# Kernel tuning notes

Hardware: AMD Instinct MI355X
Metric: run time of the kernel (lower is better)

Reference implementation:

```python
import jax, jax.numpy as jnp
import numpy as np
from jax import lax

K, E, HID, NH, L = 512, 256, 512, 8, 2
N, S1, S2, C, U, V, W = 2, 8, 9, 3, 8, 8, 8
S = S1 + S2 - 1  # 16, matches sum(cfg['seq_length']) - 1


def setup_inputs() -> dict:
    key = jax.random.key(0)
    ks = iter(jax.random.split(key, 40))
    g = lambda shape, s=0.02: jax.random.normal(next(ks), shape, jnp.float32) * s
    inp = {
        'code': jax.random.randint(next(ks), (N, S1, C, U, V, W), 0, K),
        'ncode': jax.random.randint(next(ks), (N, S2, C, U, V, W), 0, K),
        'emb': g((K, E)), 'pos_emb': g((S, E)),
        'Wq': g((L, 3, 3, 3, E, E)), 'bq': g((L, E)),
        'Wk': g((L, 3, 3, 3, E, E)), 'bk': g((L, E)),
        'Wv': g((L, 3, 3, 3, E, E)), 'bv': g((L, E)),
        'Wo': g((L, 3, 3, 3, E, E)), 'bo': g((L, E)),
        'ln1_g': jnp.ones((L, E)), 'ln1_b': jnp.zeros((L, E)),
        'ln2_g': jnp.ones((L, E)), 'ln2_b': jnp.zeros((L, E)),
        'Wc1': g((L, 3, 3, 3, E, HID)), 'bc1': g((L, HID)),
        'Wc2': g((L, 3, 3, 3, HID, E)), 'bc2': g((L, E)),
        'cls_W1': g((E, E)), 'cls_b1': jnp.zeros((E,)),
        'cls_ln_g': jnp.ones((E,)), 'cls_ln_b': jnp.zeros((E,)),
        'cls_W2': g((E, K)), 'cls_b2': jnp.zeros((K,)),
    }
    return inp


def _conv3d(t, w, b):
    # t: [B, S, U, V, W, Cin]; conv with kernel 3, stride 1, pad 1 (SAME)
    B_, S_, U_, V_, W_, Ci = t.shape
    y = lax.conv_general_dilated(t.reshape(B_ * S_, U_, V_, W_, Ci), w, (1, 1, 1), 'SAME',
                                 dimension_numbers=('NDHWC', 'DHWIO', 'NDHWC')) + b
    return y.reshape(B_, S_, U_, V_, W_, -1)


def _ln(t, g, b):
    mu = t.mean(-1, keepdims=True)
    var = ((t - mu) ** 2).mean(-1, keepdims=True)
    return (t - mu) * lax.rsqrt(var + 1e-5) * g + b


def _forward(code, ncode, emb, pos_emb, Wq, bq, Wk, bk, Wv, bv, Wo, bo,
             ln1_g, ln1_b, ln2_g, ln2_b, Wc1, bc1, Wc2, bc2,
             cls_W1, cls_b1, cls_ln_g, cls_ln_b, cls_W2, cls_b2):
    x = jnp.concatenate([code, ncode[:, :-1]], axis=1)  # [N, S, C, U, V, W]
    n, s, c, u, v, w = x.shape
    s2 = ncode.shape[1]
    x = x.transpose(0, 2, 1, 3, 4, 5).reshape(n * c, s, u, v, w)
    h = emb[x] + pos_emb[:s][None, :, None, None, None, :]  # [B, S, U, V, W, E]
    e = h.shape[-1]
    d = e // NH
    scale = jnp.asarray(d, h.dtype) ** 0.5
    # causal mask with first seq_length[0] columns fully visible
    m = jnp.tril(jnp.ones((s, s), bool)).at[:, :S1].set(True)

    def heads(t):
        return t.reshape(t.shape[0], s, u, v, w, NH, d).transpose(0, 5, 2, 3, 4, 1, 6)

    for i in range(Wq.shape[0]):
        q = heads(_conv3d(h, Wq[i], bq[i]))
        kk = heads(_conv3d(h, Wk[i], bk[i]))
        vv = heads(_conv3d(h, Wv[i], bv[i]))
        scores = jnp.einsum('bnuvwsd,bnuvwtd->bnuvwst', q, kk) / scale
        scores = jnp.where(m, scores, jnp.asarray(-1e30, scores.dtype))
        attn = jax.nn.softmax(scores, axis=-1)
        o = jnp.einsum('bnuvwst,bnuvwtd->bnuvwsd', attn, vv)
        o = o.transpose(0, 5, 2, 3, 4, 1, 6).reshape(h.shape[0], s, u, v, w, e)
        o = _conv3d(o, Wo[i], bo[i])
        h = _ln(h + o, ln1_g[i], ln1_b[i])
        f = _conv3d(jax.nn.gelu(_conv3d(h, Wc1[i], bc1[i]), approximate=False), Wc2[i], bc2[i])
        h = _ln(h + f, ln2_g[i], ln2_b[i])

    h = h[:, -s2:]
    h = h.reshape(n, c, s2, u, v, w, e).transpose(0, 2, 1, 3, 4, 5, 6)  # [N, S2, C, U, V, W, E]
    z = jnp.einsum('...e,ef->...f', h, cls_W1) + cls_b1
    z = jax.nn.gelu(_ln(z, cls_ln_g, cls_ln_b), approximate=False)
    z = jnp.einsum('...e,ek->...k', z, cls_W2) + cls_b2
    score = z.transpose(0, 6, 1, 2, 3, 4, 5)  # [N, K, S2, C, U, V, W]
    return score


def reference(code, ncode, emb, pos_emb, Wq, bq, Wk, bk, Wv, bv, Wo, bo,
              ln1_g, ln1_b, ln2_g, ln2_b, Wc1, bc1, Wc2, bc2,
              cls_W1, cls_b1, cls_ln_g, cls_ln_b, cls_W2, cls_b2):
    score = _forward(code, ncode, emb, pos_emb, Wq, bq, Wk, bk, Wv, bv, Wo, bo,
                     ln1_g, ln1_b, ln2_g, ln2_b, Wc1, bc1, Wc2, bc2,
                     cls_W1, cls_b1, cls_ln_g, cls_ln_b, cls_W2, cls_b2)
    logp = jax.nn.log_softmax(score, axis=1)
    nll = -jnp.take_along_axis(logp, ncode[:, None], axis=1)[:, 0]
    loss = nll.mean()
    pred = jnp.argmax(score, axis=1)
    return score, loss, pred
```

## Files before the change

### kernel.cpp

```cpp
#include <hip/hip_runtime.h>


typedef _Float16 f16;
typedef __attribute__((ext_vector_type(8))) _Float16 f16x8;
typedef __attribute__((ext_vector_type(4))) _Float16 f16x4;
typedef __attribute__((ext_vector_type(4))) float f32x4;

static constexpr long kSC = 14155776;
static constexpr float kDS = 4.8828125e-4f;

#define MFMA16(a, b, c) __builtin_amdgcn_mfma_f32_16x16x32_f16((a), (b), (c), 0, 0, 0)

__device__ __forceinline__ void gl16(const void* g, void* l) {
  __builtin_amdgcn_global_load_lds((const __attribute__((address_space(1))) void*)g,
                                   (__attribute__((address_space(3))) void*)l,
                                   16, 0, 0);
}

__device__ __forceinline__ float wave_sum_f(float x) {
#pragma unroll
  for (int m = 32; m; m >>= 1) x += __shfl_xor(x, m);
  return x;
}

__device__ __forceinline__ void split2(float x, f16* h, f16* l) {
  f16 hh = (f16)x;
  *h = hh;
  *l = (f16)((x - (float)hh) * 2048.0f);
}

__device__ __forceinline__ float rec2(f16 h, f16 l) {
  return (float)h + (float)l * kDS;
}

__device__ __forceinline__ float gelu_exact(float x) {
  return 0.5f * x * (1.0f + erff(x * 0.70710678118654752f));
}

__global__ __launch_bounds__(256) void wsplit_kernel(
    const float* __restrict__ src, f16* __restrict__ hi, f16* __restrict__ lo,
    int G, int Ci, int Co, int CoTot, int co0) {
  long n = (long)G * Ci * Co;
  long i = (long)blockIdx.x * 256 + threadIdx.x;
  if (i >= n) return;
  int co = (int)(i % Co);
  long t = i / Co;
  int ci = (int)(t % Ci);
  int g  = (int)(t / Ci);
  float x = src[i];
  long o = ((long)g * CoTot + co0 + co) * Ci + ci;
  split2(x, hi + o, lo + o);
}

__global__ __launch_bounds__(256) void bpack_kernel(
    const float* __restrict__ bq, const float* __restrict__ bk,
    const float* __restrict__ bv, float* __restrict__ dst) {
  int i = blockIdx.x * 256 + threadIdx.x;
  if (i < 256) dst[i] = bq[i];
  else if (i < 512) dst[i] = bk[i - 256];
  else if (i < 768) dst[i] = bv[i - 512];
}

__global__ __launch_bounds__(256) void embed_kernel(
    const int* __restrict__ code, const int* __restrict__ ncode,
    const float* __restrict__ emb, const float* __restrict__ pos,
    f16* __restrict__ Hh, f16* __restrict__ Hl) {
  int tok = blockIdx.x;
  int e = threadIdx.x;
  int g = tok >> 13;
  int rem = tok & 8191;
  int s = rem >> 9;
  int vox = rem & 511;
  int n = g / 3, c = g - 3 * n;
  int idx;
  if (s < 8) idx = code[((n * 8 + s) * 3 + c) * 512 + vox];
  else       idx = ncode[((n * 9 + (s - 8)) * 3 + c) * 512 + vox];
  float val = emb[idx * 256 + e] + pos[s * 256 + e];
  long o = (long)tok * 256 + e;
  split2(val, Hh + o, Hl + o);
}

template <int CIN, int COUTT, int ACT, int RESID>
__global__ __launch_bounds__(256, 2) void conv4_kernel(
    const f16* __restrict__ Xh, const f16* __restrict__ Xl, long xz_s, int xr,
    const f16* __restrict__ Wh, const f16* __restrict__ Wl,
    const float* __restrict__ bias,
    f16* __restrict__ Yh, f16* __restrict__ Yl, long yz_s, int yr, int nz) {
  constexpr int KB = CIN / 32;
  constexpr int NY = COUTT / 128;
  __shared__ __align__(16) f16 lsAll[32768];

  const int nwg = 64 * NY * nz;
  const int q = nwg >> 3;
  const int bid = blockIdx.x;
  const int wg = (bid & 7) * q + (bid >> 3);
  const int y = wg / (64 * nz);
  const int rem = wg - y * (64 * nz);
  const int z = rem >> 6;
  const int mt = rem & 63;
  const int img = mt >> 2, up = mt & 3;
  const int u0 = up * 2;
  const int coutb0 = y * 128;

  const int tid = threadIdx.x;
  const int wid = tid >> 6, lane = tid & 63;
  const int wm = wid >> 1, wn = wid & 1;
  const int l15 = lane & 15, lk = lane >> 4;

  const long xz = (long)z * xz_s;
  const long yz = (long)z * yz_s;

  f32x4 aA[4][4], aB[4][4];
#pragma unroll
  for (int mf = 0; mf < 4; ++mf)
#pragma unroll
    for (int nf = 0; nf < 4; ++nf) {
      float bv = bias[coutb0 + wn * 64 + nf * 16 + l15];
      aA[mf][nf] = (f32x4){bv, bv, bv, bv};
      aB[mf][nf] = (f32x4){0.f, 0.f, 0.f, 0.f};
    }

  const int swrow = tid >> 2;
  const int sslot = tid & 3;
  const int sswz = sslot ^ ((tid >> 3) & 3);

  auto stageA = [&](int kb) {
#pragma unroll
    for (int j = 0; j < 4; ++j) {
      const int uu = u0 - 1 + j;
      if (uu < 0 || uu >= 8) continue;
      const long g = xz + ((long)(img * 512 + uu * 64 + swrow)) * (long)xr
                     + kb * 32 + sswz * 8;
      gl16(Xh + g, &lsAll[j * 2048 + tid * 8]);
      gl16(Xl + g, &lsAll[8192 + j * 2048 + tid * 8]);
    }
  };
  auto stageB = [&](int o, int kb, int buf) {
#pragma unroll
    for (int i = 0; i < 2; ++i) {
      const long g = ((long)o * COUTT + coutb0 + i * 64 + swrow) * (long)CIN
                     + kb * 32 + sswz * 8;
      gl16(Wh + g, &lsAll[16384 + (buf * 2 + 0) * 4096 + i * 2048 + tid * 8]);
      gl16(Wl + g, &lsAll[16384 + (buf * 2 + 1) * 4096 + i * 2048 + tid * 8]);
    }
  };
  auto compute = [&](int o, int buf) {
    const int du = o / 9 - 1, dv = (o / 3) % 3 - 1, dw = o % 3 - 1;
    f16x8 bh[4], bl[4];
#pragma unroll
    for (int nf = 0; nf < 4; ++nf) {
      const int rb = wn * 64 + nf * 16 + l15;
      const int sw = lk ^ ((rb >> 1) & 3);
      bh[nf] = *(const f16x8*)&lsAll[16384 + (buf * 2 + 0) * 4096 + rb * 32 + sw * 8];
      bl[nf] = *(const f16x8*)&lsAll[16384 + (buf * 2 + 1) * 4096 + rb * 32 + sw * 8];
    }
    const int gu = u0 + wm + du;
    const bool uok = (0 <= gu) && (gu < 8);
    const int p = wm + 1 + du;
#pragma unroll
    for (int mf = 0; mf < 4; ++mf) {
      const int vrow = mf * 16 + l15;
      const int vv = (vrow >> 3) + dv, ww = (vrow & 7) + dw;
      const bool ok = uok && ((unsigned)vv < 8u) && ((unsigned)ww < 8u);
      f16x8 ah = {0, 0, 0, 0, 0, 0, 0, 0};
      f16x8 al = {0, 0, 0, 0, 0, 0, 0, 0};
      if (ok) {
        const int lrow = p * 64 + vv * 8 + ww;
        const int sw = lk ^ ((lrow >> 1) & 3);
        ah = *(const f16x8*)&lsAll[lrow * 32 + sw * 8];
        al = *(const f16x8*)&lsAll[8192 + lrow * 32 + sw * 8];
      }
#pragma unroll
      for (int nf = 0; nf < 4; ++nf) {
        aA[mf][nf] = MFMA16(ah, bh[nf], aA[mf][nf]);
        aB[mf][nf] = MFMA16(ah, bl[nf], aB[mf][nf]);
        aB[mf][nf] = MFMA16(al, bh[nf], aB[mf][nf]);
      }
    }
  };

  stageA(0);
  stageB(0, 0, 0);
  __syncthreads();

  int cur = 0;
#pragma unroll 1
  for (int kb = 0; kb < KB; ++kb) {
#pragma unroll 1
    for (int o = 0; o < 27; ++o) {
      if (o < 26)           stageB(o + 1, kb, cur ^ 1);
      else if (kb + 1 < KB) stageB(0, kb + 1, cur ^ 1);
      compute(o, cur);
      __syncthreads();
      cur ^= 1;
    }
    if (kb + 1 < KB) {
      stageA(kb + 1);
      __syncthreads();
    }
  }

  float* sY = (float*)lsAll;
#pragma unroll 1
  for (int rh = 0; rh < 2; ++rh) {
    if (wm == rh) {
#pragma unroll
      for (int mf = 0; mf < 4; ++mf)
#pragma unroll
        for (int nf = 0; nf < 4; ++nf)
#pragma unroll
          for (int j = 0; j < 4; ++j) {
            const int row = mf * 16 + lk * 4 + j;
            const int col = wn * 64 + nf * 16 + l15;
            sY[row * 132 + col] = aA[mf][nf][j] + aB[mf][nf][j] * kDS;
          }
    }
    __syncthreads();
#pragma unroll
    for (int it = 0; it < 2; ++it) {
      const int row = it * 32 + (tid >> 3);
      const int c0 = (tid & 7) * 16;
      const long grow = (long)img * 512 + (u0 + rh) * 64 + row;
      const long gidx = yz + grow * (long)yr + coutb0 + c0;
      float yv[16];
#pragma unroll
      for (int i2 = 0; i2 < 16; ++i2) yv[i2] = sY[row * 132 + c0 + i2];
      if (ACT) {
#pragma unroll
        for (int i2 = 0; i2 < 16; ++i2) yv[i2] = gelu_exact(yv[i2]);
      }
      if (RESID) {
        f16x8 r0h = *(const f16x8*)&Yh[gidx];
        f16x8 r1h = *(const f16x8*)&Yh[gidx + 8];
        f16x8 r0l = *(const f16x8*)&Yl[gidx];
        f16x8 r1l = *(const f16x8*)&Yl[gidx + 8];
#pragma unroll
        for (int i2 = 0; i2 < 8; ++i2) {
          yv[i2] += rec2(r0h[i2], r0l[i2]);
          yv[8 + i2] += rec2(r1h[i2], r1l[i2]);
        }
      }
      f16x8 h0, h1, l0, l1;
#pragma unroll
      for (int i2 = 0; i2 < 8; ++i2) {
        f16 a, b;
        split2(yv[i2], &a, &b); h0[i2] = a; l0[i2] = b;
        split2(yv[8 + i2], &a, &b); h1[i2] = a; l1[i2] = b;
      }
      *(f16x8*)&Yh[gidx] = h0;
      *(f16x8*)&Yh[gidx + 8] = h1;
      *(f16x8*)&Yl[gidx] = l0;
      *(f16x8*)&Yl[gidx + 8] = l1;
    }
    __syncthreads();
  }
}

template <int K_, int COUT, bool F32OUT>
__global__ __launch_bounds__(256) void gemm_kernel(
    const f16* __restrict__ Xh, const f16* __restrict__ Xl,
    const f16* __restrict__ Wh, const f16* __restrict__ Wl,
    const float* __restrict__ bias,
    f16* __restrict__ Yh, f16* __restrict__ Yl, float* __restrict__ Yf) {
  const int m0 = blockIdx.x * 64;
  const int coutb = blockIdx.y * 64;
  const int tid = threadIdx.x;
  const int wid = tid >> 6, lane = tid & 63;
  const int l15 = lane & 15, lk = lane >> 4;
  const int arow = m0 + wid * 16 + l15;

  f32x4 accA[4], accB[4];
#pragma unroll
  for (int cg = 0; cg < 4; ++cg) {
    float bv = bias[coutb + cg * 16 + l15];
    accA[cg] = (f32x4){bv, bv, bv, bv};
    accB[cg] = (f32x4){0.f, 0.f, 0.f, 0.f};
  }
  const f16* pah = Xh + (long)arow * K_ + lk * 8;
  const f16* pal = Xl + (long)arow * K_ + lk * 8;
  const f16* pbh = Wh + ((long)coutb + l15) * K_ + lk * 8;
  const f16* pbl = Wl + ((long)coutb + l15) * K_ + lk * 8;
#pragma unroll 2
  for (int kb = 0; kb < K_ / 32; ++kb) {
    f16x8 ah = *(const f16x8*)(pah + kb * 32);
    f16x8 al = *(const f16x8*)(pal + kb * 32);
#pragma unroll
    for (int cg = 0; cg < 4; ++cg) {
      f16x8 bh = *(const f16x8*)(pbh + (long)cg * 16 * K_ + kb * 32);
      f16x8 bl = *(const f16x8*)(pbl + (long)cg * 16 * K_ + kb * 32);
      accA[cg] = MFMA16(ah, bh, accA[cg]);
      accB[cg] = MFMA16(ah, bl, accB[cg]);
      accB[cg] = MFMA16(al, bh, accB[cg]);
    }
  }
  const long ybase = ((long)m0 + wid * 16) * (long)COUT + coutb;
#pragma unroll
  for (int cg = 0; cg < 4; ++cg)
#pragma unroll
    for (int j = 0; j < 4; ++j) {
      int r = lk * 4 + j;
      float y = accA[cg][j] + accB[cg][j] * kDS;
      long idx = ybase + (long)r * COUT + cg * 16 + l15;
      if (F32OUT) Yf[idx] = y;
      else        split2(y, Yh + idx, Yl + idx);
    }
}

__global__ __launch_bounds__(256) void attn_kernel(
    f16* __restrict__ QKVh, f16* __restrict__ QKVl) {
  __shared__ float sq[4][16][33];
  __shared__ float sk[4][16][33];
  __shared__ float sv[4][16][33];
  __shared__ float ss[4][16][17];
  const int wid = threadIdx.x >> 6, lane = threadIdx.x & 63;
  const int p = blockIdx.x * 4 + wid;
  const int cs = p >> 12;
  const int loc = p & 4095;
  const int nh = loc >> 9;
  const int vox = loc & 511;
  const int srow = lane >> 2;
  const int dp = (lane & 3) * 8;
  const long sbase = (long)cs * 6291456;
  const long base = sbase + ((long)(srow * 512 + vox)) * 768 + nh * 32 + dp;

  {
    f16x8 qh = *(const f16x8*)(QKVh + base);
    f16x8 ql = *(const f16x8*)(QKVl + base);
    f16x8 kh = *(const f16x8*)(QKVh + base + 256);
    f16x8 kl = *(const f16x8*)(QKVl + base + 256);
    f16x8 vh = *(const f16x8*)(QKVh + base + 512);
    f16x8 vl = *(const f16x8*)(QKVl + base + 512);
#pragma unroll
    for (int j = 0; j < 8; ++j) {
      sq[wid][srow][dp + j] = rec2(qh[j], ql[j]);
      sk[wid][srow][dp + j] = rec2(kh[j], kl[j]);
      sv[wid][srow][dp + j] = rec2(vh[j], vl[j]);
    }
  }
  __syncthreads();
#pragma unroll
  for (int pp = 0; pp < 4; ++pp) {
    int pr = lane * 4 + pp;
    int qi = pr >> 4, kt = pr & 15;
    float s = 0.f;
#pragma unroll
    for (int d = 0; d < 32; ++d) s += sq[wid][qi][d] * sk[wid][kt][d];
    bool allowed = (kt < 8) || (kt <= qi);
    ss[wid][qi][kt] = allowed ? s * 0.17677669529663687f : -1e30f;
  }
  __syncthreads();
  if (lane < 16) {
    float m = -1e30f;
#pragma unroll
    for (int t = 0; t < 16; ++t) m = fmaxf(m, ss[wid][lane][t]);
    float ex[16];
    float sum = 0.f;
#pragma unroll
    for (int t = 0; t < 16; ++t) { ex[t] = expf(ss[wid][lane][t] - m); sum += ex[t]; }
    float inv = 1.0f / sum;
#pragma unroll
    for (int t = 0; t < 16; ++t) ss[wid][lane][t] = ex[t] * inv;
  }
  __syncthreads();
  float o[8] = {0, 0, 0, 0, 0, 0, 0, 0};
#pragma unroll
  for (int t = 0; t < 16; ++t) {
    float a = ss[wid][srow][t];
#pragma unroll
    for (int j = 0; j < 8; ++j) o[j] += a * sv[wid][t][dp + j];
  }
#pragma unroll
  for (int j = 0; j < 8; ++j) split2(o[j], QKVh + base + j, QKVl + base + j);
}

__global__ __launch_bounds__(256) void ln_kernel(
    f16* __restrict__ Hh, f16* __restrict__ Hl,
    const float* __restrict__ gam, const float* __restrict__ bet) {
  const int wid = threadIdx.x >> 6, lane = threadIdx.x & 63;
  const long tok = (long)blockIdx.x * 4 + wid;
  const long base = tok * 256 + lane * 4;
  f16x4 hh = *(const f16x4*)(Hh + base);
  f16x4 hl = *(const f16x4*)(Hl + base);
  float v0 = rec2(hh[0], hl[0]), v1 = rec2(hh[1], hl[1]);
  float v2 = rec2(hh[2], hl[2]), v3 = rec2(hh[3], hl[3]);
  float mu = wave_sum_f(v0 + v1 + v2 + v3) * (1.0f / 256.0f);
  float d0 = v0 - mu, d1 = v1 - mu, d2 = v2 - mu, d3 = v3 - mu;
  float var = wave_sum_f(d0 * d0 + d1 * d1 + d2 * d2 + d3 * d3) * (1.0f / 256.0f);
  float rs = rsqrtf(var + 1e-5f);
  float4 gv = *(const float4*)(gam + lane * 4);
  float4 bv = *(const float4*)(bet + lane * 4);
  float y0 = d0 * rs * gv.x + bv.x, y1 = d1 * rs * gv.y + bv.y;
  float y2 = d2 * rs * gv.z + bv.z, y3 = d3 * rs * gv.w + bv.w;
  f16x4 oh, ol;
  f16 a, b2;
  split2(y0, &a, &b2); oh[0] = a; ol[0] = b2;
  split2(y1, &a, &b2); oh[1] = a; ol[1] = b2;
  split2(y2, &a, &b2); oh[2] = a; ol[2] = b2;
  split2(y3, &a, &b2); oh[3] = a; ol[3] = b2;
  *(f16x4*)(Hh + base) = oh;
  *(f16x4*)(Hl + base) = ol;
}

__global__ __launch_bounds__(256) void ln_gelu_kernel(
    f16* __restrict__ Zh, f16* __restrict__ Zl,
    const float* __restrict__ gam, const float* __restrict__ bet) {
  const int wid = threadIdx.x >> 6, lane = threadIdx.x & 63;
  const long tok = (long)blockIdx.x * 4 + wid;
  const long base = tok * 256 + lane * 4;
  f16x4 hh = *(const f16x4*)(Zh + base);
  f16x4 hl = *(const f16x4*)(Zl + base);
  float v0 = rec2(hh[0], hl[0]), v1 = rec2(hh[1], hl[1]);
  float v2 = rec2(hh[2], hl[2]), v3 = rec2(hh[3], hl[3]);
  float mu = wave_sum_f(v0 + v1 + v2 + v3) * (1.0f / 256.0f);
  float d0 = v0 - mu, d1 = v1 - mu, d2 = v2 - mu, d3 = v3 - mu;
  float var = wave_sum_f(d0 * d0 + d1 * d1 + d2 * d2 + d3 * d3) * (1.0f / 256.0f);
  float rs = rsqrtf(var + 1e-5f);
  float4 gv = *(const float4*)(gam + lane * 4);
  float4 bv = *(const float4*)(bet + lane * 4);
  float y0 = gelu_exact(d0 * rs * gv.x + bv.x);
  float y1 = gelu_exact(d1 * rs * gv.y + bv.y);
  float y2 = gelu_exact(d2 * rs * gv.z + bv.z);
  float y3 = gelu_exact(d3 * rs * gv.w + bv.w);
  f16x4 oh, ol;
  f16 a, b2;
  split2(y0, &a, &b2); oh[0] = a; ol[0] = b2;
  split2(y1, &a, &b2); oh[1] = a; ol[1] = b2;
  split2(y2, &a, &b2); oh[2] = a; ol[2] = b2;
  split2(y3, &a, &b2); oh[3] = a; ol[3] = b2;
  *(f16x4*)(Zh + base) = oh;
  *(f16x4*)(Zl + base) = ol;
}

__global__ __launch_bounds__(256) void gather_kernel(
    const f16* __restrict__ Hh, const f16* __restrict__ Hl, int n,
    f16* __restrict__ Xh, f16* __restrict__ Xl) {
  const int tc = blockIdx.x;
  const int e = threadIdx.x;
  const int s2 = tc / 1536;
  int r = tc - s2 * 1536;
  const int c = r >> 9;
  const int vox = r & 511;
  const int g = n * 3 + c;
  const int s = 7 + s2;
  const long src = ((long)(g * 16 + s) * 512 + vox) * 256 + e;
  const long dst = (long)tc * 256 + e;
  Xh[dst] = Hh[src];
  Xl[dst] = Hl[src];
}

__global__ __launch_bounds__(256) void transpose_kernel(
    const float* __restrict__ Z2, float* __restrict__ out) {
  __shared__ float tile[32][33];
  const int t0 = blockIdx.x * 32;
  const int k0 = blockIdx.y * 32;
  const int tx = threadIdx.x & 31;
  const int ty = threadIdx.x >> 5;
#pragma unroll
  for (int i = 0; i < 32; i += 8)
    tile[ty + i][tx] = Z2[((long)(t0 + ty + i)) * 512 + k0 + tx];
  __syncthreads();
#pragma unroll
  for (int i = 0; i < 32; i += 8)
    out[((long)(k0 + ty + i)) * 13824 + t0 + tx] = tile[tx][ty + i];
}

__global__ __launch_bounds__(256) void loss_pred_kernel(
    const float* __restrict__ Z2, const int* __restrict__ ncode,
    float* __restrict__ pred, float* __restrict__ partial) {
  __shared__ float sh[4];
  const int wid = threadIdx.x >> 6, lane = threadIdx.x & 63;
  const int tok = blockIdx.x * 4 + wid;
  const float* row = Z2 + (long)tok * 512;
  float4 a = *(const float4*)(row + lane * 8);
  float4 b = *(const float4*)(row + lane * 8 + 4);
  float vals[8] = {a.x, a.y, a.z, a.w, b.x, b.y, b.z, b.w};
  float mx = vals[0];
  int mi = lane * 8;
#pragma unroll
  for (int j = 1; j < 8; ++j)
    if (vals[j] > mx) { mx = vals[j]; mi = lane * 8 + j; }
#pragma unroll
  for (int m = 1; m < 64; m <<= 1) {
    float ox = __shfl_xor(mx, m);
    int oi = __shfl_xor(mi, m);
    if (ox > mx || (ox == mx && oi < mi)) { mx = ox; mi = oi; }
  }
  float se = 0.f;
#pragma unroll
  for (int j = 0; j < 8; ++j) se += expf(vals[j] - mx);
  se = wave_sum_f(se);
  if (lane == 0) {
    int tgt = ncode[tok];
    float nll = mx + logf(se) - row[tgt];
    pred[tok] = (float)mi;
    sh[wid] = nll;
  }
  __syncthreads();
  if (threadIdx.x == 0) partial[blockIdx.x] = sh[0] + sh[1] + sh[2] + sh[3];
}

__global__ __launch_bounds__(256) void loss_final_kernel(
    const float* __restrict__ partial, float* __restrict__ out) {
  __shared__ float sh[4];
  float s = 0.f;
  for (int i = threadIdx.x; i < 6912; i += 256) s += partial[i];
  s = wave_sum_f(s);
  if ((threadIdx.x & 63) == 0) sh[threadIdx.x >> 6] = s;
  __syncthreads();
  if (threadIdx.x == 0) out[0] = (sh[0] + sh[1] + sh[2] + sh[3]) * (1.0f / 27648.0f);
}

__global__ __launch_bounds__(256) void fill_kernel(float* __restrict__ p, long n, float v) {
  long i = (long)blockIdx.x * 256 + threadIdx.x;
  if (i < n) p[i] = v;
}

extern "C" void kernel_launch(void* const* d_in, const int* in_sizes, int n_in,
                              void* d_out, int out_size, void* d_ws, size_t ws_size,
                              hipStream_t stream) {
  const int* code   = (const int*)d_in[0];
  const int* ncode  = (const int*)d_in[1];
  const float* emb  = (const float*)d_in[2];
  const float* pos  = (const float*)d_in[3];
  const float* Wq   = (const float*)d_in[4];
  const float* bq   = (const float*)d_in[5];
  const float* Wk   = (const float*)d_in[6];
  const float* bk   = (const float*)d_in[7];
  const float* Wv   = (const float*)d_in[8];
  const float* bv   = (const float*)d_in[9];
  const float* Wo   = (const float*)d_in[10];
  const float* bo   = (const float*)d_in[11];
  const float* ln1g = (const float*)d_in[12];
  const float* ln1b = (const float*)d_in[13];
  const float* ln2g = (const float*)d_in[14];
  const float* ln2b = (const float*)d_in[15];
  const float* Wc1  = (const float*)d_in[16];
  const float* bc1  = (const float*)d_in[17];
  const float* Wc2  = (const float*)d_in[18];
  const float* bc2  = (const float*)d_in[19];
  const float* cW1  = (const float*)d_in[20];
  const float* cb1  = (const float*)d_in[21];
  const float* clng = (const float*)d_in[22];
  const float* clnb = (const float*)d_in[23];
  const float* cW2  = (const float*)d_in[24];
  const float* cb2  = (const float*)d_in[25];
  float* out = (float*)d_out;
  (void)in_sizes; (void)n_in; (void)out_size;

  const long WSLOT = 5308416;
  const long HSL   = 2097152;
  const long QSL   = 6291456;
  const long T1SL  = 4194304;
  const long CLMIN = 21233664;

  auto needf = [&](int ns) -> size_t {
    long slab = (long)ns * 2 * QSL;
    if (slab < CLMIN) slab = CLMIN;
    return (size_t)(2 * WSLOT + 2 * 12582912L + slab) * 2 + 6912 * 4 + 768 * 4 + 4096;
  };
  int NS = 0;
  if      (ws_size >= needf(6)) NS = 6;
  else if (ws_size >= needf(3)) NS = 3;
  else if (ws_size >= needf(2)) NS = 2;
  else if (ws_size >= needf(1)) NS = 1;
  if (NS == 0) {
    fill_kernel<<<dim3(109), 256, 0, stream>>>(out + kSC, 27649, -1.0f);
    return;
  }
  long slab_f16 = (long)NS * 2 * QSL;
  if (slab_f16 < CLMIN) slab_f16 = CLMIN;

  f16* wh = (f16*)d_ws;
  f16* wl = wh + WSLOT;
  f16* Hh = wl + WSLOT;
  f16* Hl = Hh + 12582912;
  f16* S  = Hl + 12582912;
  float* partial = (float*)(S + slab_f16);
  float* bcat = partial + 6912;

  const size_t WQKVO = 27u * 256 * 256;
  const size_t WC1SZ = 27u * 256 * 512;
  const size_t WC2SZ = 27u * 512 * 256;

  embed_kernel<<<dim3(49152), 256, 0, stream>>>(code, ncode, emb, pos, Hh, Hl);

  const int nchunk = 6 / NS;
  f16* qkvh = S;
  f16* qkvl = S + (long)NS * QSL;
  f16* t1h  = S;
  f16* t1l  = S + (long)NS * T1SL;

  for (int l = 0; l < 2; ++l) {
    const float* wq = Wq + (size_t)l * WQKVO;
    const float* wk = Wk + (size_t)l * WQKVO;
    const float* wv = Wv + (size_t)l * WQKVO;
    const float* wo = Wo + (size_t)l * WQKVO;
    const float* wc1 = Wc1 + (size_t)l * WC1SZ;
    const float* wc2 = Wc2 + (size_t)l * WC2SZ;
    bpack_kernel<<<dim3(3), 256, 0, stream>>>(bq + l * 256, bk + l * 256, bv + l * 256, bcat);
    for (int ch = 0; ch < nchunk; ++ch) {
      f16* Xh = Hh + (long)ch * NS * HSL;
      f16* Xl = Hl + (long)ch * NS * HSL;
      wsplit_kernel<<<dim3(6912), 256, 0, stream>>>(wq, wh, wl, 27, 256, 256, 768, 0);
      wsplit_kernel<<<dim3(6912), 256, 0, stream>>>(wk, wh, wl, 27, 256, 256, 768, 256);
      wsplit_kernel<<<dim3(6912), 256, 0, stream>>>(wv, wh, wl, 27, 256, 256, 768, 512);
      conv4_kernel<256, 768, 0, 0><<<dim3(64 * 6 * NS), 256, 0, stream>>>(
          Xh, Xl, HSL, 256, wh, wl, bcat, qkvh, qkvl, QSL, 768, NS);
      attn_kernel<<<dim3(NS * 1024), 256, 0, stream>>>(qkvh, qkvl);
      wsplit_kernel<<<dim3(6912), 256, 0, stream>>>(wo, wh, wl, 27, 256, 256, 256, 0);
      conv4_kernel<256, 256, 0, 1><<<dim3(64 * 2 * NS), 256, 0, stream>>>(
          qkvh, qkvl, QSL, 768, wh, wl, bo + l * 256, Xh, Xl, HSL, 256, NS);
      ln_kernel<<<dim3(2048 * NS), 256, 0, stream>>>(Xh, Xl, ln1g + l * 256, ln1b + l * 256);
      wsplit_kernel<<<dim3(13824), 256, 0, stream>>>(wc1, wh, wl, 27, 256, 512, 512, 0);
      conv4_kernel<256, 512, 1, 0><<<dim3(64 * 4 * NS), 256, 0, stream>>>(
          Xh, Xl, HSL, 256, wh, wl, bc1 + l * 512, t1h, t1l, T1SL, 512, NS);
      wsplit_kernel<<<dim3(13824), 256, 0, stream>>>(wc2, wh, wl, 27, 512, 256, 256, 0);
      conv4_kernel<512, 256, 0, 1><<<dim3(64 * 2 * NS), 256, 0, stream>>>(
          t1h, t1l, T1SL, 512, wh, wl, bc2 + l * 256, Xh, Xl, HSL, 256, NS);
      ln_kernel<<<dim3(2048 * NS), 256, 0, stream>>>(Xh, Xl, ln2g + l * 256, ln2b + l * 256);
    }
  }

  for (int n = 0; n < 2; ++n) {
    f16* Z1h = S;
    f16* Z1l = S + 3538944;
    f16* Xch = S + 7077888;
    f16* Xcl = S + 10616832;
    float* Z2 = (float*)(S + 7077888);
    gather_kernel<<<dim3(13824), 256, 0, stream>>>(Hh, Hl, n, Xch, Xcl);
    wsplit_kernel<<<dim3(256), 256, 0, stream>>>(cW1, wh, wl, 1, 256, 256, 256, 0);
    gemm_kernel<256, 256, false><<<dim3(216, 4), 256, 0, stream>>>(Xch, Xcl, wh, wl, cb1, Z1h, Z1l, nullptr);
    ln_gelu_kernel<<<dim3(3456), 256, 0, stream>>>(Z1h, Z1l, clng, clnb);
    wsplit_kernel<<<dim3(512), 256, 0, stream>>>(cW2, wh, wl, 1, 256, 512, 512, 0);
    gemm_kernel<256, 512, true><<<dim3(216, 8), 256, 0, stream>>>(Z1h, Z1l, wh, wl, cb2, nullptr, nullptr, Z2);
    transpose_kernel<<<dim3(432, 16), 256, 0, stream>>>(Z2, out + (long)n * 512 * 13824);
    loss_pred_kernel<<<dim3(3456), 256, 0, stream>>>(Z2, ncode + n * 13824,
                                                     out + kSC + 1 + n * 13824, partial + n * 3456);
  }
  loss_final_kernel<<<dim3(1), 256, 0, stream>>>(partial, out + kSC);
}
```

Baseline: 7.532 ms.

## Refine conv pipeline with fine-grained waits, skip out-of-range taps, setprio

Replaces the full __syncthreads in the conv kernel's K-loop with explicit vmcnt waits and raw barriers, so the next weight tile's loads stay in flight while the current tile is computed. Waves whose tap falls outside the u range now skip the whole compute step, including the B fragment loads. The loop also raises wave priority around the MFMA block, prefetches B together with the next A stage, and uses nontemporal stores for non-residual outputs. The hand-written waitcnt counts assume a fixed number of outstanding loads per thread, which is fragile if the compiler reorders memory operations or the load count per stage changes.

```diff
diff --git a/kernel.cpp b/kernel.cpp
--- a/kernel.cpp
+++ b/kernel.cpp
@@ -81,7 +81,7 @@
 }
 
 template <int CIN, int COUTT, int ACT, int RESID>
-__global__ __launch_bounds__(256, 2) void conv4_kernel(
+__global__ __launch_bounds__(256, 2) void conv5_kernel(
     const f16* __restrict__ Xh, const f16* __restrict__ Xl, long xz_s, int xr,
     const f16* __restrict__ Wh, const f16* __restrict__ Wl,
     const float* __restrict__ bias,
@@ -146,6 +146,9 @@
   };
   auto compute = [&](int o, int buf) {
     const int du = o / 9 - 1, dv = (o / 3) % 3 - 1, dw = o % 3 - 1;
+    const int gu = u0 + wm + du;
+    if ((unsigned)gu >= 8u) return;
+    const int p = wm + 1 + du;
     f16x8 bh[4], bl[4];
 #pragma unroll
     for (int nf = 0; nf < 4; ++nf) {
@@ -154,14 +157,12 @@
       bh[nf] = *(const f16x8*)&lsAll[16384 + (buf * 2 + 0) * 4096 + rb * 32 + sw * 8];
       bl[nf] = *(const f16x8*)&lsAll[16384 + (buf * 2 + 1) * 4096 + rb * 32 + sw * 8];
     }
-    const int gu = u0 + wm + du;
-    const bool uok = (0 <= gu) && (gu < 8);
-    const int p = wm + 1 + du;
+    __builtin_amdgcn_s_setprio(1);
 #pragma unroll
     for (int mf = 0; mf < 4; ++mf) {
       const int vrow = mf * 16 + l15;
       const int vv = (vrow >> 3) + dv, ww = (vrow & 7) + dw;
-      const bool ok = uok && ((unsigned)vv < 8u) && ((unsigned)ww < 8u);
+      const bool ok = ((unsigned)vv < 8u) && ((unsigned)ww < 8u);
       f16x8 ah = {0, 0, 0, 0, 0, 0, 0, 0};
       f16x8 al = {0, 0, 0, 0, 0, 0, 0, 0};
       if (ok) {
@@ -177,26 +178,31 @@
         aB[mf][nf] = MFMA16(al, bh[nf], aB[mf][nf]);
       }
     }
+    __builtin_amdgcn_s_setprio(0);
   };
 
   stageA(0);
   stageB(0, 0, 0);
   __syncthreads();
 
-  int cur = 0;
 #pragma unroll 1
   for (int kb = 0; kb < KB; ++kb) {
 #pragma unroll 1
     for (int o = 0; o < 27; ++o) {
-      if (o < 26)           stageB(o + 1, kb, cur ^ 1);
-      else if (kb + 1 < KB) stageB(0, kb + 1, cur ^ 1);
+      const int cur = o & 1;
+      if (o < 26) {
+        stageB(o + 1, kb, cur ^ 1);
+        asm volatile("s_waitcnt vmcnt(4)\n\ts_barrier" ::: "memory");
+      } else {
+        asm volatile("s_waitcnt vmcnt(0)\n\ts_barrier" ::: "memory");
+      }
       compute(o, cur);
-      __syncthreads();
-      cur ^= 1;
+      asm volatile("s_barrier" ::: "memory");
     }
     if (kb + 1 < KB) {
       stageA(kb + 1);
-      __syncthreads();
+      stageB(0, kb + 1, 0);
+      asm volatile("s_waitcnt vmcnt(0)\n\ts_barrier" ::: "memory");
     }
   }
 
@@ -247,10 +253,17 @@
         split2(yv[i2], &a, &b); h0[i2] = a; l0[i2] = b;
         split2(yv[8 + i2], &a, &b); h1[i2] = a; l1[i2] = b;
       }
-      *(f16x8*)&Yh[gidx] = h0;
-      *(f16x8*)&Yh[gidx + 8] = h1;
-      *(f16x8*)&Yl[gidx] = l0;
-      *(f16x8*)&Yl[gidx + 8] = l1;
+      if (RESID) {
+        *(f16x8*)&Yh[gidx] = h0;
+        *(f16x8*)&Yh[gidx + 8] = h1;
+        *(f16x8*)&Yl[gidx] = l0;
+        *(f16x8*)&Yl[gidx + 8] = l1;
+      } else {
+        __builtin_nontemporal_store(h0, (f16x8*)&Yh[gidx]);
+        __builtin_nontemporal_store(h1, (f16x8*)&Yh[gidx + 8]);
+        __builtin_nontemporal_store(l0, (f16x8*)&Yl[gidx]);
+        __builtin_nontemporal_store(l1, (f16x8*)&Yl[gidx + 8]);
+      }
     }
     __syncthreads();
   }
@@ -604,18 +617,18 @@
       wsplit_kernel<<<dim3(6912), 256, 0, stream>>>(wq, wh, wl, 27, 256, 256, 768, 0);
       wsplit_kernel<<<dim3(6912), 256, 0, stream>>>(wk, wh, wl, 27, 256, 256, 768, 256);
       wsplit_kernel<<<dim3(6912), 256, 0, stream>>>(wv, wh, wl, 27, 256, 256, 768, 512);
-      conv4_kernel<256, 768, 0, 0><<<dim3(64 * 6 * NS), 256, 0, stream>>>(
+      conv5_kernel<256, 768, 0, 0><<<dim3(64 * 6 * NS), 256, 0, stream>>>(
           Xh, Xl, HSL, 256, wh, wl, bcat, qkvh, qkvl, QSL, 768, NS);
       attn_kernel<<<dim3(NS * 1024), 256, 0, stream>>>(qkvh, qkvl);
       wsplit_kernel<<<dim3(6912), 256, 0, stream>>>(wo, wh, wl, 27, 256, 256, 256, 0);
-      conv4_kernel<256, 256, 0, 1><<<dim3(64 * 2 * NS), 256, 0, stream>>>(
+      conv5_kernel<256, 256, 0, 1><<<dim3(64 * 2 * NS), 256, 0, stream>>>(
           qkvh, qkvl, QSL, 768, wh, wl, bo + l * 256, Xh, Xl, HSL, 256, NS);
       ln_kernel<<<dim3(2048 * NS), 256, 0, stream>>>(Xh, Xl, ln1g + l * 256, ln1b + l * 256);
       wsplit_kernel<<<dim3(13824), 256, 0, stream>>>(wc1, wh, wl, 27, 256, 512, 512, 0);
-      conv4_kernel<256, 512, 1, 0><<<dim3(64 * 4 * NS), 256, 0, stream>>>(
+      conv5_kernel<256, 512, 1, 0><<<dim3(64 * 4 * NS), 256, 0, stream>>>(
           Xh, Xl, HSL, 256, wh, wl, bc1 + l * 512, t1h, t1l, T1SL, 512, NS);
       wsplit_kernel<<<dim3(13824), 256, 0, stream>>>(wc2, wh, wl, 27, 512, 256, 256, 0);
-      conv4_kernel<512, 256, 0, 1><<<dim3(64 * 2 * NS), 256, 0, stream>>>(
+      conv5_kernel<512, 256, 0, 1><<<dim3(64 * 2 * NS), 256, 0, stream>>>(
           t1h, t1l, T1SL, 512, wh, wl, bc2 + l * 256, Xh, Xl, HSL, 256, NS);
       ln_kernel<<<dim3(2048 * NS), 256, 0, stream>>>(Xh, Xl, ln2g + l * 256, ln2b + l * 256);
     }
```

After: 7.505 ms. About the same (-0.4%).

## Halve conv output tile to 64 channels, raise occupancy, skip out-of-range depth taps

Applied to the files above, without the earlier changes.

The implicit-GEMM conv kernel now computes 64 output channels per workgroup instead of 128. This halves the accumulator registers and shrinks shared memory, so launch bounds can ask for 3 workgroups per CU, and the grid doubles. Compute now returns early for taps whose depth index falls outside the volume, raises wave priority around the MFMA block, and uses nontemporal stores for non-residual outputs. In exchange, each input A tile is restaged twice as often across workgroups, which lowers data reuse and adds global/LDS traffic.

```diff
diff --git a/kernel.cpp b/kernel.cpp
--- a/kernel.cpp
+++ b/kernel.cpp
@@ -81,14 +81,14 @@
 }
 
 template <int CIN, int COUTT, int ACT, int RESID>
-__global__ __launch_bounds__(256, 2) void conv4_kernel(
+__global__ __launch_bounds__(256, 3) void conv12_kernel(
     const f16* __restrict__ Xh, const f16* __restrict__ Xl, long xz_s, int xr,
     const f16* __restrict__ Wh, const f16* __restrict__ Wl,
     const float* __restrict__ bias,
     f16* __restrict__ Yh, f16* __restrict__ Yl, long yz_s, int yr, int nz) {
   constexpr int KB = CIN / 32;
-  constexpr int NY = COUTT / 128;
-  __shared__ __align__(16) f16 lsAll[32768];
+  constexpr int NY = COUTT / 64;
+  __shared__ __align__(16) f16 lsAll[24576];
 
   const int nwg = 64 * NY * nz;
   const int q = nwg >> 3;
@@ -100,7 +100,7 @@
   const int mt = rem & 63;
   const int img = mt >> 2, up = mt & 3;
   const int u0 = up * 2;
-  const int coutb0 = y * 128;
+  const int coutb0 = y * 64;
 
   const int tid = threadIdx.x;
   const int wid = tid >> 6, lane = tid & 63;
@@ -110,19 +110,18 @@
   const long xz = (long)z * xz_s;
   const long yz = (long)z * yz_s;
 
-  f32x4 aA[4][4], aB[4][4];
+  f32x4 aA[4][2], aB[4][2];
 #pragma unroll
   for (int mf = 0; mf < 4; ++mf)
 #pragma unroll
-    for (int nf = 0; nf < 4; ++nf) {
-      float bv = bias[coutb0 + wn * 64 + nf * 16 + l15];
+    for (int nf = 0; nf < 2; ++nf) {
+      float bv = bias[coutb0 + wn * 32 + nf * 16 + l15];
       aA[mf][nf] = (f32x4){bv, bv, bv, bv};
       aB[mf][nf] = (f32x4){0.f, 0.f, 0.f, 0.f};
     }
 
   const int swrow = tid >> 2;
-  const int sslot = tid & 3;
-  const int sswz = sslot ^ ((tid >> 3) & 3);
+  const int sswz = (tid & 3) ^ ((tid >> 3) & 3);
 
   auto stageA = [&](int kb) {
 #pragma unroll
@@ -136,32 +135,32 @@
     }
   };
   auto stageB = [&](int o, int kb, int buf) {
-#pragma unroll
-    for (int i = 0; i < 2; ++i) {
-      const long g = ((long)o * COUTT + coutb0 + i * 64 + swrow) * (long)CIN
-                     + kb * 32 + sswz * 8;
-      gl16(Wh + g, &lsAll[16384 + (buf * 2 + 0) * 4096 + i * 2048 + tid * 8]);
-      gl16(Wl + g, &lsAll[16384 + (buf * 2 + 1) * 4096 + i * 2048 + tid * 8]);
-    }
+    const int wb = 16384 + buf * 4096;
+    const long g = ((long)o * COUTT + coutb0 + swrow) * (long)CIN
+                   + kb * 32 + sswz * 8;
+    gl16(Wh + g, &lsAll[wb + tid * 8]);
+    gl16(Wl + g, &lsAll[wb + 2048 + tid * 8]);
   };
   auto compute = [&](int o, int buf) {
     const int du = o / 9 - 1, dv = (o / 3) % 3 - 1, dw = o % 3 - 1;
-    f16x8 bh[4], bl[4];
-#pragma unroll
-    for (int nf = 0; nf < 4; ++nf) {
-      const int rb = wn * 64 + nf * 16 + l15;
+    const int gu = u0 + wm + du;
+    if ((unsigned)gu >= 8u) return;
+    const int p = wm + 1 + du;
+    const int wb = 16384 + buf * 4096;
+    f16x8 bh[2], bl[2];
+#pragma unroll
+    for (int nf = 0; nf < 2; ++nf) {
+      const int rb = wn * 32 + nf * 16 + l15;
       const int sw = lk ^ ((rb >> 1) & 3);
-      bh[nf] = *(const f16x8*)&lsAll[16384 + (buf * 2 + 0) * 4096 + rb * 32 + sw * 8];
-      bl[nf] = *(const f16x8*)&lsAll[16384 + (buf * 2 + 1) * 4096 + rb * 32 + sw * 8];
-    }
-    const int gu = u0 + wm + du;
-    const bool uok = (0 <= gu) && (gu < 8);
-    const int p = wm + 1 + du;
+      bh[nf] = *(const f16x8*)&lsAll[wb + rb * 32 + sw * 8];
+      bl[nf] = *(const f16x8*)&lsAll[wb + 2048 + rb * 32 + sw * 8];
+    }
+    __builtin_amdgcn_s_setprio(1);
 #pragma unroll
     for (int mf = 0; mf < 4; ++mf) {
       const int vrow = mf * 16 + l15;
       const int vv = (vrow >> 3) + dv, ww = (vrow & 7) + dw;
-      const bool ok = uok && ((unsigned)vv < 8u) && ((unsigned)ww < 8u);
+      const bool ok = ((unsigned)vv < 8u) && ((unsigned)ww < 8u);
       f16x8 ah = {0, 0, 0, 0, 0, 0, 0, 0};
       f16x8 al = {0, 0, 0, 0, 0, 0, 0, 0};
       if (ok) {
@@ -171,12 +170,13 @@
         al = *(const f16x8*)&lsAll[8192 + lrow * 32 + sw * 8];
       }
 #pragma unroll
-      for (int nf = 0; nf < 4; ++nf) {
+      for (int nf = 0; nf < 2; ++nf) {
         aA[mf][nf] = MFMA16(ah, bh[nf], aA[mf][nf]);
         aB[mf][nf] = MFMA16(ah, bl[nf], aB[mf][nf]);
         aB[mf][nf] = MFMA16(al, bh[nf], aB[mf][nf]);
       }
     }
+    __builtin_amdgcn_s_setprio(0);
   };
 
   stageA(0);
@@ -207,50 +207,47 @@
 #pragma unroll
       for (int mf = 0; mf < 4; ++mf)
 #pragma unroll
-        for (int nf = 0; nf < 4; ++nf)
+        for (int nf = 0; nf < 2; ++nf)
 #pragma unroll
           for (int j = 0; j < 4; ++j) {
             const int row = mf * 16 + lk * 4 + j;
-            const int col = wn * 64 + nf * 16 + l15;
-            sY[row * 132 + col] = aA[mf][nf][j] + aB[mf][nf][j] * kDS;
+            const int col = wn * 32 + nf * 16 + l15;
+            sY[row * 68 + col] = aA[mf][nf][j] + aB[mf][nf][j] * kDS;
           }
     }
     __syncthreads();
 #pragma unroll
     for (int it = 0; it < 2; ++it) {
       const int row = it * 32 + (tid >> 3);
-      const int c0 = (tid & 7) * 16;
+      const int c0 = (tid & 7) * 8;
       const long grow = (long)img * 512 + (u0 + rh) * 64 + row;
       const long gidx = yz + grow * (long)yr + coutb0 + c0;
-      float yv[16];
-#pragma unroll
-      for (int i2 = 0; i2 < 16; ++i2) yv[i2] = sY[row * 132 + c0 + i2];
+      float yv[8];
+#pragma unroll
+      for (int i2 = 0; i2 < 8; ++i2) yv[i2] = sY[row * 68 + c0 + i2];
       if (ACT) {
 #pragma unroll
-        for (int i2 = 0; i2 < 16; ++i2) yv[i2] = gelu_exact(yv[i2]);
+        for (int i2 = 0; i2 < 8; ++i2) yv[i2] = gelu_exact(yv[i2]);
       }
       if (RESID) {
         f16x8 r0h = *(const f16x8*)&Yh[gidx];
-        f16x8 r1h = *(const f16x8*)&Yh[gidx + 8];
         f16x8 r0l = *(const f16x8*)&Yl[gidx];
-        f16x8 r1l = *(const f16x8*)&Yl[gidx + 8];
-#pragma unroll
-        for (int i2 = 0; i2 < 8; ++i2) {
-          yv[i2] += rec2(r0h[i2], r0l[i2]);
-          yv[8 + i2] += rec2(r1h[i2], r1l[i2]);
-        }
+#pragma unroll
+        for (int i2 = 0; i2 < 8; ++i2) yv[i2] += rec2(r0h[i2], r0l[i2]);
       }
-      f16x8 h0, h1, l0, l1;
+      f16x8 h0, l0;
 #pragma unroll
       for (int i2 = 0; i2 < 8; ++i2) {
         f16 a, b;
         split2(yv[i2], &a, &b); h0[i2] = a; l0[i2] = b;
-        split2(yv[8 + i2], &a, &b); h1[i2] = a; l1[i2] = b;
       }
-      *(f16x8*)&Yh[gidx] = h0;
-      *(f16x8*)&Yh[gidx + 8] = h1;
-      *(f16x8*)&Yl[gidx] = l0;
-      *(f16x8*)&Yl[gidx + 8] = l1;
+      if (RESID) {
+        *(f16x8*)&Yh[gidx] = h0;
+        *(f16x8*)&Yl[gidx] = l0;
+      } else {
+        __builtin_nontemporal_store(h0, (f16x8*)&Yh[gidx]);
+        __builtin_nontemporal_store(l0, (f16x8*)&Yl[gidx]);
+      }
     }
     __syncthreads();
   }
@@ -604,18 +601,18 @@
       wsplit_kernel<<<dim3(6912), 256, 0, stream>>>(wq, wh, wl, 27, 256, 256, 768, 0);
       wsplit_kernel<<<dim3(6912), 256, 0, stream>>>(wk, wh, wl, 27, 256, 256, 768, 256);
       wsplit_kernel<<<dim3(6912), 256, 0, stream>>>(wv, wh, wl, 27, 256, 256, 768, 512);
-      conv4_kernel<256, 768, 0, 0><<<dim3(64 * 6 * NS), 256, 0, stream>>>(
+      conv12_kernel<256, 768, 0, 0><<<dim3(64 * 12 * NS), 256, 0, stream>>>(
           Xh, Xl, HSL, 256, wh, wl, bcat, qkvh, qkvl, QSL, 768, NS);
       attn_kernel<<<dim3(NS * 1024), 256, 0, stream>>>(qkvh, qkvl);
       wsplit_kernel<<<dim3(6912), 256, 0, stream>>>(wo, wh, wl, 27, 256, 256, 256, 0);
-      conv4_kernel<256, 256, 0, 1><<<dim3(64 * 2 * NS), 256, 0, stream>>>(
+      conv12_kernel<256, 256, 0, 1><<<dim3(64 * 4 * NS), 256, 0, stream>>>(
           qkvh, qkvl, QSL, 768, wh, wl, bo + l * 256, Xh, Xl, HSL, 256, NS);
       ln_kernel<<<dim3(2048 * NS), 256, 0, stream>>>(Xh, Xl, ln1g + l * 256, ln1b + l * 256);
       wsplit_kernel<<<dim3(13824), 256, 0, stream>>>(wc1, wh, wl, 27, 256, 512, 512, 0);
-      conv4_kernel<256, 512, 1, 0><<<dim3(64 * 4 * NS), 256, 0, stream>>>(
+      conv12_kernel<256, 512, 1, 0><<<dim3(64 * 8 * NS), 256, 0, stream>>>(
           Xh, Xl, HSL, 256, wh, wl, bc1 + l * 512, t1h, t1l, T1SL, 512, NS);
       wsplit_kernel<<<dim3(13824), 256, 0, stream>>>(wc2, wh, wl, 27, 512, 256, 256, 0);
-      conv4_kernel<512, 256, 0, 1><<<dim3(64 * 2 * NS), 256, 0, stream>>>(
+      conv12_kernel<512, 256, 0, 1><<<dim3(64 * 4 * NS), 256, 0, stream>>>(
           t1h, t1l, T1SL, 512, wh, wl, bc2 + l * 256, Xh, Xl, HSL, 256, NS);
       ln_kernel<<<dim3(2048 * NS), 256, 0, stream>>>(Xh, Xl, ln2g + l * 256, ln2b + l * 256);
     }
```

Result: slower. 7.756 ms (+3.0%).
